# Optimization experiments

Measured on AMD Instinct MI355X. Metric: run time of the kernel, lower is better.

Reference implementation:

```python
import jax, jax.numpy as jnp
import numpy as np

B, T, TKV, D, H = 4, 2048, 512, 1024, 16
HD = D // H  # 64
HIDDEN = ((int(D * 4 * 2 / 3) + 7) // 8) * 8  # 2736
EPS = 1e-6


def setup_inputs() -> dict:
    key = jax.random.key(0)
    ks = jax.random.split(key, 16)
    x = jax.random.normal(ks[0], (B, T, D), jnp.float32)
    memory = jax.random.normal(ks[1], (B, TKV, D), jnp.float32)
    # RoPE frequencies: (T, HD//2, 2) = (cos, sin)
    inv_freq = 1.0 / (10000.0 ** (jnp.arange(0, HD, 2, dtype=jnp.float32) / HD))
    angles = jnp.arange(T, dtype=jnp.float32)[:, None] * inv_freq[None, :]
    freqs_cis = jnp.stack([jnp.cos(angles), jnp.sin(angles)], axis=-1)
    # causal mask (T, T): 0 on/below diag, -inf above
    causal_mask = jnp.where(jnp.tril(jnp.ones((T, T), bool)), 0.0, -jnp.inf).astype(jnp.float32)
    s = 0.02
    w = lambda k, i, o: jax.random.normal(k, (i, o), jnp.float32) * s  # stored as (in, out)
    return {
        'x': x, 'memory': memory, 'freqs_cis': freqs_cis, 'causal_mask': causal_mask,
        'sa_wq': w(ks[2], D, D), 'sa_wk': w(ks[3], D, D), 'sa_wv': w(ks[4], D, D), 'sa_wo': w(ks[5], D, D),
        'ca_wq': w(ks[6], D, D), 'ca_wk': w(ks[7], D, D), 'ca_wv': w(ks[8], D, D), 'ca_wo': w(ks[9], D, D),
        'w1': w(ks[10], D, HIDDEN), 'w3': w(ks[11], D, HIDDEN), 'w2': w(ks[12], HIDDEN, D),
        'g_sa': jnp.ones((D,), jnp.float32), 'g_ca': jnp.ones((D,), jnp.float32), 'g_ffn': jnp.ones((D,), jnp.float32),
    }


def rmsnorm(x, g):
    return x * jax.lax.rsqrt(jnp.mean(x * x, axis=-1, keepdims=True) + EPS) * g


def apply_rope(t, f):
    # t: (B, H, T, HD); f: (T, HD//2, 2)
    tr = t.reshape(*t.shape[:-1], HD // 2, 2)
    a, b = tr[..., 0], tr[..., 1]
    cos, sin = f[None, None, :, :, 0], f[None, None, :, :, 1]
    out = jnp.stack([a * cos - b * sin, a * sin + b * cos], axis=-1)
    return out.reshape(t.shape)


def heads(x, w):
    # (B, S, D) @ (D, D) -> (B, H, S, HD)
    b, s, _ = x.shape
    return (x @ w).reshape(b, s, H, HD).transpose(0, 2, 1, 3)


def attention(xq, kv, wq, wk, wv, wo, freqs=None, mask=None):
    q, k, v = heads(xq, wq), heads(kv, wk), heads(kv, wv)
    if freqs is not None:
        q, k = apply_rope(q, freqs), apply_rope(k, freqs)
    attn = jnp.einsum('bhqd,bhkd->bhqk', q, k) * (HD ** -0.5)
    if mask is not None:
        attn = attn + mask
    attn = jax.nn.softmax(attn, axis=-1)
    out = jnp.einsum('bhqk,bhkd->bhqd', attn, v)
    out = out.transpose(0, 2, 1, 3).reshape(xq.shape[0], xq.shape[1], D)
    return out @ wo


def reference(x, memory, freqs_cis, causal_mask,
              sa_wq, sa_wk, sa_wv, sa_wo,
              ca_wq, ca_wk, ca_wv, ca_wo,
              w1, w2, w3, g_sa, g_ca, g_ffn):
    x = rmsnorm(x + attention(x, x, sa_wq, sa_wk, sa_wv, sa_wo, freqs=freqs_cis, mask=causal_mask), g_sa)
    x = rmsnorm(x + attention(x, memory, ca_wq, ca_wk, ca_wv, ca_wo), g_ca)
    ffn = (jax.nn.silu(x @ w1) * (x @ w3)) @ w2
    x = rmsnorm(x + ffn, g_ffn)
    return x
```

## Files before the change

kernel.cpp:

```cpp
#include <hip/hip_runtime.h>
#include <hip/hip_bf16.h>

typedef __attribute__((ext_vector_type(8))) short s16x8;
typedef __attribute__((ext_vector_type(4))) float f32x4;
typedef __attribute__((ext_vector_type(16))) float f32x16;
typedef unsigned short u16;
typedef unsigned int u32;
typedef unsigned long long u64;

#define MFMA(a,b,c) __builtin_amdgcn_mfma_f32_16x16x32_bf16(a,b,c,0,0,0)
#define MFMA32(a,b,c) __builtin_amdgcn_mfma_f32_32x32x16_bf16(a,b,c,0,0,0)

constexpr int B_ = 4, T_ = 2048, TKV_ = 512, D_ = 1024, H_ = 16, HD_ = 64;
constexpr int HID_ = 2736, HIDP_ = 2816;

__device__ __forceinline__ float bf2f(u16 x) {
    union { float f; u32 u; } c; c.u = ((u32)x) << 16; return c.f;
}
__device__ __forceinline__ u16 f2bf(float f) {
    union { float f; u32 u; } c; c.f = f;
    u32 r = c.u + 0x7fffu + ((c.u >> 16) & 1u);
    return (u16)(r >> 16);
}

__device__ __forceinline__ void gload16(const void* g, void* l) {
    __builtin_amdgcn_global_load_lds(
        (const __attribute__((address_space(1))) u32*)g,
        (__attribute__((address_space(3))) u32*)l, 16, 0, 0);
}

__global__ __launch_bounds__(256) void wt_cast(const float* __restrict__ W, u16* __restrict__ WT,
                                               int K, int N, int Kp, int Np) {
    __shared__ float t[32][33];
    int tid = threadIdx.x;
    int tx = tid & 31, ty = tid >> 5;
    int n0 = blockIdx.x * 32, k0 = blockIdx.y * 32;
#pragma unroll
    for (int i = 0; i < 4; ++i) {
        int kk = k0 + ty + i * 8, nn = n0 + tx;
        t[ty + i * 8][tx] = (kk < K && nn < N) ? W[(size_t)kk * N + nn] : 0.f;
    }
    __syncthreads();
#pragma unroll
    for (int i = 0; i < 4; ++i) {
        int nn = n0 + ty + i * 8, kk = k0 + tx;
        WT[(size_t)nn * Kp + kk] = f2bf(t[tx][ty + i * 8]);
    }
}

__global__ __launch_bounds__(256) void cast_bf16(const float* __restrict__ in, u16* __restrict__ out, int n4) {
    int i = blockIdx.x * 256 + threadIdx.x;
    if (i >= n4) return;
    float4 v = ((const float4*)in)[i];
    u64 pk = (u64)f2bf(v.x) | ((u64)f2bf(v.y) << 16) | ((u64)f2bf(v.z) << 32) | ((u64)f2bf(v.w) << 48);
    ((u64*)out)[i] = pk;
}

__device__ __forceinline__ void gemm_store(void* C, const u16* mul, size_t idx, float v, int mode) {
    if (mode == 0) {
        ((float*)C)[idx] = v;
    } else if (mode == 1) {
        ((u16*)C)[idx] = f2bf(v);
    } else if (mode == 2) {
        float sg = 1.f / (1.f + __expf(-v));
        ((u16*)C)[idx] = f2bf(v * sg);
    } else if (mode == 3) {
        float h = bf2f(mul[idx]);
        ((u16*)C)[idx] = f2bf(v * h);
    } else {
        ((u16*)C)[idx] = f2bf(v * 0.125f);
    }
}


__global__ __launch_bounds__(256) void gemm_bf16(const u16* __restrict__ A, const u16* __restrict__ Bt,
                                                 void* __restrict__ C, const u16* __restrict__ mul,
                                                 int M, int N, int K, int mode, int nwg) {
    __shared__ __align__(16) u16 As[128 * 64];
    __shared__ __align__(16) u16 Bs[128 * 64];
    const int tid = threadIdx.x;
    const int lane = tid & 63, wid = tid >> 6;
    const int wr = wid >> 1, wc = wid & 1;
    const int li = lane & 15, g = lane >> 4;

    int bid = (int)blockIdx.x;
    bid = (bid & 7) * (nwg >> 3) + (bid >> 3);

    const int tn = N >> 7;
    const int m0 = (bid / tn) * 128, n0 = (bid % tn) * 128;

    const int rowst = tid >> 3;
    const int colb = (((tid & 7) ^ ((tid >> 3) & 7)) * 16);
    const char* ga = (const char*)A + ((size_t)(m0 + rowst) * K) * 2 + colb;
    const char* gb = (const char*)Bt + ((size_t)(n0 + rowst) * K) * 2 + colb;
    const size_t rstride = (size_t)32 * K * 2;

    f32x4 acc[4][4] = {};
    const int nt = K >> 6;

    for (int t = 0; t < nt; ++t) {
#pragma unroll
        for (int i = 0; i < 4; ++i) {
            gload16(ga + (size_t)t * 128 + i * rstride, (char*)As + i * 4096 + wid * 1024);
            gload16(gb + (size_t)t * 128 + i * rstride, (char*)Bs + i * 4096 + wid * 1024);
        }
        __syncthreads();
#pragma unroll
        for (int kk = 0; kk < 2; ++kk) {
            s16x8 aF[4], bF[4];
            const int sl = ((kk << 2) | g) ^ (li & 7);
#pragma unroll
            for (int m = 0; m < 4; ++m) aF[m] = *(const s16x8*)&As[(wr * 64 + m * 16 + li) * 64 + sl * 8];
#pragma unroll
            for (int n = 0; n < 4; ++n) bF[n] = *(const s16x8*)&Bs[(wc * 64 + n * 16 + li) * 64 + sl * 8];
#pragma unroll
            for (int m = 0; m < 4; ++m)
#pragma unroll
                for (int n = 0; n < 4; ++n)
                    acc[m][n] = MFMA(aF[m], bF[n], acc[m][n]);
        }
        __syncthreads();
    }

#pragma unroll
    for (int m = 0; m < 4; ++m)
#pragma unroll
        for (int n = 0; n < 4; ++n)
#pragma unroll
            for (int r = 0; r < 4; ++r) {
                size_t row = m0 + wr * 64 + m * 16 + g * 4 + r;
                size_t col = n0 + wc * 64 + n * 16 + li;
                gemm_store(C, mul, row * N + col, acc[m][n][r], mode);
            }
}

__global__ __launch_bounds__(256) void gemm_w13(const u16* __restrict__ A, const u16* __restrict__ B1t,
                                                const u16* __restrict__ B3t, u16* __restrict__ Hout,
                                                int M, int N, int K, int nwg) {
    __shared__ __align__(16) u16 As[128 * 64];
    __shared__ __align__(16) u16 B1s[128 * 64];
    __shared__ __align__(16) u16 B3s[128 * 64];
    const int tid = threadIdx.x;
    const int lane = tid & 63, wid = tid >> 6;
    const int wr = wid >> 1, wc = wid & 1;
    const int li = lane & 15, g = lane >> 4;

    int bid = (int)blockIdx.x;
    bid = (bid & 7) * (nwg >> 3) + (bid >> 3);

    const int tn = N >> 7;
    const int m0 = (bid / tn) * 128, n0 = (bid % tn) * 128;

    const int rowst = tid >> 3;
    const int colb = (((tid & 7) ^ ((tid >> 3) & 7)) * 16);
    const char* ga = (const char*)A + ((size_t)(m0 + rowst) * K) * 2 + colb;
    const char* gb1 = (const char*)B1t + ((size_t)(n0 + rowst) * K) * 2 + colb;
    const char* gb3 = (const char*)B3t + ((size_t)(n0 + rowst) * K) * 2 + colb;
    const size_t rstride = (size_t)32 * K * 2;

    f32x4 acc1[4][4] = {}, acc3[4][4] = {};
    const int nt = K >> 6;

    for (int t = 0; t < nt; ++t) {
#pragma unroll
        for (int i = 0; i < 4; ++i) {
            gload16(ga + (size_t)t * 128 + i * rstride, (char*)As + i * 4096 + wid * 1024);
            gload16(gb1 + (size_t)t * 128 + i * rstride, (char*)B1s + i * 4096 + wid * 1024);
            gload16(gb3 + (size_t)t * 128 + i * rstride, (char*)B3s + i * 4096 + wid * 1024);
        }
        __syncthreads();
#pragma unroll
        for (int kk = 0; kk < 2; ++kk) {
            const int sl = ((kk << 2) | g) ^ (li & 7);
            s16x8 aF[4];
#pragma unroll
            for (int m = 0; m < 4; ++m) aF[m] = *(const s16x8*)&As[(wr * 64 + m * 16 + li) * 64 + sl * 8];
            {
                s16x8 bF[4];
#pragma unroll
                for (int n = 0; n < 4; ++n) bF[n] = *(const s16x8*)&B1s[(wc * 64 + n * 16 + li) * 64 + sl * 8];
#pragma unroll
                for (int m = 0; m < 4; ++m)
#pragma unroll
                    for (int n = 0; n < 4; ++n)
                        acc1[m][n] = MFMA(aF[m], bF[n], acc1[m][n]);
            }
            {
                s16x8 bF[4];
#pragma unroll
                for (int n = 0; n < 4; ++n) bF[n] = *(const s16x8*)&B3s[(wc * 64 + n * 16 + li) * 64 + sl * 8];
#pragma unroll
                for (int m = 0; m < 4; ++m)
#pragma unroll
                    for (int n = 0; n < 4; ++n)
                        acc3[m][n] = MFMA(aF[m], bF[n], acc3[m][n]);
            }
        }
        __syncthreads();
    }

#pragma unroll
    for (int m = 0; m < 4; ++m)
#pragma unroll
        for (int n = 0; n < 4; ++n)
#pragma unroll
            for (int r = 0; r < 4; ++r) {
                size_t row = m0 + wr * 64 + m * 16 + g * 4 + r;
                size_t col = n0 + wc * 64 + n * 16 + li;
                float h1 = acc1[m][n][r];
                float h3 = acc3[m][n][r];
                float sg = 1.f / (1.f + __expf(-h1));
                Hout[row * N + col] = f2bf(h1 * sg * h3);
            }
}

__global__ __launch_bounds__(256) void rope_qk(u16* __restrict__ q, u16* __restrict__ k,
                                               const float* __restrict__ fr, int S) {
    size_t idx = (size_t)blockIdx.x * 256 + threadIdx.x;
    int i = (int)(idx & 31);
    int h = (int)((idx >> 5) & 15);
    size_t bt = idx >> 9;
    int t = (int)(bt & (T_ - 1));
    float2 cs = ((const float2*)fr)[t * 32 + i];
    size_t off = bt * (size_t)S + h * 64 + 2 * i;
    {
        u32* p = (u32*)(q + off);
        u32 w = *p;
        float a = bf2f((u16)(w & 0xffff)), b = bf2f((u16)(w >> 16));
        *p = (u32)f2bf((a * cs.x - b * cs.y) * 0.125f) | ((u32)f2bf((a * cs.y + b * cs.x) * 0.125f) << 16);
    }
    {
        u32* p = (u32*)(k + off);
        u32 w = *p;
        float a = bf2f((u16)(w & 0xffff)), b = bf2f((u16)(w >> 16));
        *p = (u32)f2bf(a * cs.x - b * cs.y) | ((u32)f2bf(a * cs.y + b * cs.x) << 16);
    }
}

__global__ __launch_bounds__(256) void vtrans(const u16* __restrict__ v, u16* __restrict__ vT,
                                              int Tk, int S) {
    __shared__ u16 tile[32][34];
    int bh = blockIdx.x;
    int t0 = blockIdx.y * 32, d0 = blockIdx.z * 32;
    int b = bh >> 4, h = bh & 15;
    int tid = threadIdx.x;
    int tx = tid & 31, ty = tid >> 5;
#pragma unroll
    for (int i = 0; i < 4; ++i)
        tile[ty + i * 8][tx] = v[((size_t)b * Tk + t0 + ty + i * 8) * S + h * 64 + d0 + tx];
    __syncthreads();
#pragma unroll
    for (int i = 0; i < 4; ++i)
        vT[((size_t)bh * 64 + d0 + ty + i * 8) * Tk + t0 + tx] = tile[tx][ty + i * 8];
}

__device__ __forceinline__ void attn32(const u16* __restrict__ qh, const u16* __restrict__ kh,
                                       const u16* __restrict__ vh, u16* __restrict__ oh,
                                       int q0, int nkb, int Tk, int causal, int lq, int hi,
                                       int QS, int KS) {
    const u16* qb = qh + (size_t)(q0 + lq) * QS;
    s16x8 qf[4];
#pragma unroll
    for (int c = 0; c < 4; ++c) qf[c] = *(const s16x8*)&qb[c * 16 + hi * 8];

    f32x16 o0 = {}, o1 = {};
    float mr = -1e30f, lr = 0.f;

    for (int kb = 0; kb < nkb; ++kb) {
        const int ks = kb * 32;
        f32x16 s = {};
        const u16* kp = kh + (size_t)(ks + lq) * KS + hi * 8;
#pragma unroll
        for (int c = 0; c < 4; ++c) {
            s16x8 kf = *(const s16x8*)&kp[c * 16];
            s = MFMA32(kf, qf[c], s);
        }
        if (causal && kb == nkb - 1) {
#pragma unroll
            for (int r = 0; r < 16; ++r) {
                int kl = (r & 3) + 8 * (r >> 2) + 4 * hi;
                if (kl > lq) s[r] = -1e30f;
            }
        }
        float bm = fmaxf(fmaxf(fmaxf(s[0], s[1]), fmaxf(s[2], s[3])),
                         fmaxf(fmaxf(s[4], s[5]), fmaxf(s[6], s[7])));
        float bm2 = fmaxf(fmaxf(fmaxf(s[8], s[9]), fmaxf(s[10], s[11])),
                          fmaxf(fmaxf(s[12], s[13]), fmaxf(s[14], s[15])));
        bm = fmaxf(bm, bm2);
        bm = fmaxf(bm, __shfl_xor(bm, 32));
        float mn = fmaxf(mr, bm);
        float sc = __expf(mr - mn);
        mr = mn;
        float p[16];
        float rs = 0.f;
#pragma unroll
        for (int r = 0; r < 16; ++r) { p[r] = __expf(s[r] - mn); rs += p[r]; }
        rs += __shfl_xor(rs, 32);
        lr = lr * sc + rs;
#pragma unroll
        for (int r = 0; r < 16; ++r) { o0[r] *= sc; o1[r] *= sc; }

        u32 pk[8];
#pragma unroll
        for (int i = 0; i < 8; ++i)
            pk[i] = (u32)f2bf(p[2 * i]) | ((u32)f2bf(p[2 * i + 1]) << 16);
        u32 e1 = __shfl_xor(hi ? pk[0] : pk[2], 32);
        u32 e2 = __shfl_xor(hi ? pk[1] : pk[3], 32);
        u32 e3 = __shfl_xor(hi ? pk[4] : pk[6], 32);
        u32 e4 = __shfl_xor(hi ? pk[5] : pk[7], 32);
        union { s16x8 v; u32 w[4]; } pf0, pf1;
        pf0.w[0] = hi ? e1 : pk[0];
        pf0.w[1] = hi ? e2 : pk[1];
        pf0.w[2] = hi ? pk[2] : e1;
        pf0.w[3] = hi ? pk[3] : e2;
        pf1.w[0] = hi ? e3 : pk[4];
        pf1.w[1] = hi ? e4 : pk[5];
        pf1.w[2] = hi ? pk[6] : e3;
        pf1.w[3] = hi ? pk[7] : e4;

        const u16* v0 = vh + (size_t)lq * Tk + ks + hi * 8;
        const u16* v1 = vh + (size_t)(32 + lq) * Tk + ks + hi * 8;
        o0 = MFMA32(*(const s16x8*)&v0[0],  pf0.v, o0);
        o0 = MFMA32(*(const s16x8*)&v0[16], pf1.v, o0);
        o1 = MFMA32(*(const s16x8*)&v1[0],  pf0.v, o1);
        o1 = MFMA32(*(const s16x8*)&v1[16], pf1.v, o1);
    }

    float inv = 1.f / lr;
    u16* ob = oh + (size_t)(q0 + lq) * D_;
#pragma unroll
    for (int r = 0; r < 16; ++r) {
        int hd = (r & 3) + 8 * (r >> 2) + 4 * hi;
        ob[hd] = f2bf(o0[r] * inv);
        ob[hd + 32] = f2bf(o1[r] * inv);
    }
}

__global__ __launch_bounds__(256) void attn_causal32(const u16* __restrict__ q, const u16* __restrict__ k,
                                                     const u16* __restrict__ vT, u16* __restrict__ o,
                                                     int Tq, int Tk, int QS, int KS) {
    const int lane = threadIdx.x & 63, wid = threadIdx.x >> 6;
    const int lq = lane & 31, hi = lane >> 5;
    const int ntile = Tq / 32;
    const int ppb = (ntile / 2) / 4;
    const int bh = blockIdx.x / ppb;
    const int p = (blockIdx.x % ppb) * 4 + wid;
    const int b = bh >> 4, h = bh & 15;

    const u16* qh = q + ((size_t)b * Tq) * QS + h * 64;
    const u16* kh = k + ((size_t)b * Tk) * KS + h * 64;
    const u16* vh = vT + ((size_t)bh * 64) * Tk;
    u16* oh = o + ((size_t)b * Tq) * D_ + h * 64;

    const int tA = p, tB = ntile - 1 - p;
    attn32(qh, kh, vh, oh, tA * 32, tA + 1, Tk, 1, lq, hi, QS, KS);
    attn32(qh, kh, vh, oh, tB * 32, tB + 1, Tk, 1, lq, hi, QS, KS);
}

__global__ __launch_bounds__(256) void attn_plain32(const u16* __restrict__ q, const u16* __restrict__ k,
                                                    const u16* __restrict__ vT, u16* __restrict__ o,
                                                    int Tq, int Tk, int QS, int KS) {
    const int lane = threadIdx.x & 63, wid = threadIdx.x >> 6;
    const int lq = lane & 31, hi = lane >> 5;
    const int tpb = (Tq / 32) / 4;
    const int bh = blockIdx.x / tpb;
    const int qt = (blockIdx.x % tpb) * 4 + wid;
    const int b = bh >> 4, h = bh & 15;

    const u16* qh = q + ((size_t)b * Tq) * QS + h * 64;
    const u16* kh = k + ((size_t)b * Tk) * KS + h * 64;
    const u16* vh = vT + ((size_t)bh * 64) * Tk;
    u16* oh = o + ((size_t)b * Tq) * D_ + h * 64;

    attn32(qh, kh, vh, oh, qt * 32, Tk / 32, Tk, 0, lq, hi, QS, KS);
}

__global__ __launch_bounds__(256) void addnorm(const float* __restrict__ xa, const float* __restrict__ xb,
                                               const float* __restrict__ gg, float* __restrict__ fo,
                                               u16* __restrict__ bo) {
    int row = blockIdx.x * 4 + (threadIdx.x >> 6);
    int lane = threadIdx.x & 63;
    const float4* pa = (const float4*)(xa + (size_t)row * D_);
    const float4* pb = (const float4*)(xb + (size_t)row * D_);
    float4 v[4];
    float ss = 0.f;
#pragma unroll
    for (int j = 0; j < 4; ++j) {
        float4 a = pa[lane + 64 * j];
        float4 b = pb[lane + 64 * j];
        v[j].x = a.x + b.x; v[j].y = a.y + b.y; v[j].z = a.z + b.z; v[j].w = a.w + b.w;
        ss += v[j].x * v[j].x + v[j].y * v[j].y + v[j].z * v[j].z + v[j].w * v[j].w;
    }
    ss += __shfl_xor(ss, 1);
    ss += __shfl_xor(ss, 2);
    ss += __shfl_xor(ss, 4);
    ss += __shfl_xor(ss, 8);
    ss += __shfl_xor(ss, 16);
    ss += __shfl_xor(ss, 32);
    float s = rsqrtf(ss * (1.0f / D_) + 1e-6f);
#pragma unroll
    for (int j = 0; j < 4; ++j) {
        float4 gv = ((const float4*)gg)[lane + 64 * j];
        float yx = v[j].x * s * gv.x, yy = v[j].y * s * gv.y;
        float yz = v[j].z * s * gv.z, yw = v[j].w * s * gv.w;
        if (fo) {
            float4 o4; o4.x = yx; o4.y = yy; o4.z = yz; o4.w = yw;
            ((float4*)(fo + (size_t)row * D_))[lane + 64 * j] = o4;
        }
        if (bo) {
            u64 pk = (u64)f2bf(yx) | ((u64)f2bf(yy) << 16) | ((u64)f2bf(yz) << 32) | ((u64)f2bf(yw) << 48);
            ((u64*)(bo + (size_t)row * D_))[lane + 64 * j] = pk;
        }
    }
}

extern "C" void kernel_launch(void* const* d_in, const int* in_sizes, int n_in,
                              void* d_out, int out_size, void* d_ws, size_t ws_size,
                              hipStream_t stream) {
    const float* x    = (const float*)d_in[0];
    const float* mem  = (const float*)d_in[1];
    const float* fr   = (const float*)d_in[2];
    const float* wsaq = (const float*)d_in[4];
    const float* wsak = (const float*)d_in[5];
    const float* wsav = (const float*)d_in[6];
    const float* wsao = (const float*)d_in[7];
    const float* wcaq = (const float*)d_in[8];
    const float* wcak = (const float*)d_in[9];
    const float* wcav = (const float*)d_in[10];
    const float* wcao = (const float*)d_in[11];
    const float* w1   = (const float*)d_in[12];
    const float* w3   = (const float*)d_in[13];
    const float* w2   = (const float*)d_in[14];
    const float* g_sa = (const float*)d_in[15];
    const float* g_ca = (const float*)d_in[16];
    const float* g_ff = (const float*)d_in[17];
    float* outF = (float*)d_out;

    char* p = (char*)d_ws;
    auto alloc = [&](size_t bytes) { char* r = p; p += (bytes + 255) & ~(size_t)255; return r; };
    const size_t DD2 = (size_t)1024 * 1024 * 2;
    u16* wqkvT = (u16*)alloc(3 * DD2);
    u16* saoT  = (u16*)alloc(DD2);
    u16* caqT  = (u16*)alloc(DD2);
    u16* wkvT  = (u16*)alloc(2 * DD2);
    u16* caoT  = (u16*)alloc(DD2);
    u16* w1T   = (u16*)alloc((size_t)HIDP_ * 1024 * 2);
    u16* w3T   = (u16*)alloc((size_t)HIDP_ * 1024 * 2);
    u16* w2T   = (u16*)alloc((size_t)1024 * HIDP_ * 2);
    u16* Ab    = (u16*)alloc((size_t)8192 * 1024 * 2);
    u16* memb  = (u16*)alloc((size_t)2048 * 1024 * 2);
    char* qkvRaw = alloc((size_t)8192 * 3072 * 2);
    u16* qkvb = (u16*)qkvRaw;
    u16* kvb  = (u16*)qkvRaw;
    u16* caqb = (u16*)(qkvRaw + (size_t)25165824);
    u16* vtb  = (u16*)alloc((size_t)8192 * 1024 * 2);
    u16* ob   = (u16*)alloc((size_t)8192 * 1024 * 2);
    float* Pf = (float*)alloc((size_t)8192 * 1024 * 4);
    float* Rf = (float*)alloc((size_t)8192 * 1024 * 4);
    u16* Hb   = (u16*)alloc((size_t)8192 * HIDP_ * 2);

    dim3 blk(256);

    wt_cast<<<dim3(32, 32), blk, 0, stream>>>(wsaq, wqkvT,               1024, 1024, 1024, 1024);
    wt_cast<<<dim3(32, 32), blk, 0, stream>>>(wsak, wqkvT + 1024 * 1024, 1024, 1024, 1024, 1024);
    wt_cast<<<dim3(32, 32), blk, 0, stream>>>(wsav, wqkvT + 2048 * 1024, 1024, 1024, 1024, 1024);
    wt_cast<<<dim3(32, 32), blk, 0, stream>>>(wsao, saoT, 1024, 1024, 1024, 1024);
    wt_cast<<<dim3(32, 32), blk, 0, stream>>>(wcaq, caqT, 1024, 1024, 1024, 1024);
    wt_cast<<<dim3(32, 32), blk, 0, stream>>>(wcak, wkvT,               1024, 1024, 1024, 1024);
    wt_cast<<<dim3(32, 32), blk, 0, stream>>>(wcav, wkvT + 1024 * 1024, 1024, 1024, 1024, 1024);
    wt_cast<<<dim3(32, 32), blk, 0, stream>>>(wcao, caoT, 1024, 1024, 1024, 1024);
    wt_cast<<<dim3(88, 32), blk, 0, stream>>>(w1, w1T, 1024, HID_, 1024, HIDP_);
    wt_cast<<<dim3(88, 32), blk, 0, stream>>>(w3, w3T, 1024, HID_, 1024, HIDP_);
    wt_cast<<<dim3(32, 88), blk, 0, stream>>>(w2, w2T, HID_, 1024, HIDP_, 1024);

    cast_bf16<<<8192, blk, 0, stream>>>(x, Ab, 2097152);
    cast_bf16<<<2048, blk, 0, stream>>>(mem, memb, 524288);

    gemm_bf16<<<1536, blk, 0, stream>>>(Ab, wqkvT, qkvb, nullptr, 8192, 3072, 1024, 1, 1536);
    rope_qk<<<16384, blk, 0, stream>>>(qkvb, qkvb + 1024, fr, 3072);
    vtrans<<<dim3(64, 64, 2), blk, 0, stream>>>(qkvb + 2048, vtb, 2048, 3072);
    attn_causal32<<<512, blk, 0, stream>>>(qkvb, qkvb + 1024, vtb, ob, 2048, 2048, 3072, 3072);
    gemm_bf16<<<512, blk, 0, stream>>>(ob, saoT, Pf, nullptr, 8192, 1024, 1024, 0, 512);
    addnorm<<<2048, blk, 0, stream>>>(x, Pf, g_sa, Rf, Ab);

    gemm_bf16<<<512, blk, 0, stream>>>(Ab, caqT, caqb, nullptr, 8192, 1024, 1024, 4, 512);
    gemm_bf16<<<256, blk, 0, stream>>>(memb, wkvT, kvb, nullptr, 2048, 2048, 1024, 1, 256);
    vtrans<<<dim3(64, 16, 2), blk, 0, stream>>>(kvb + 1024, vtb, 512, 2048);
    attn_plain32<<<1024, blk, 0, stream>>>(caqb, kvb, vtb, ob, 2048, 512, 1024, 2048);
    gemm_bf16<<<512, blk, 0, stream>>>(ob, caoT, Pf, nullptr, 8192, 1024, 1024, 0, 512);
    addnorm<<<2048, blk, 0, stream>>>(Rf, Pf, g_ca, Rf, Ab);

    gemm_w13<<<1408, blk, 0, stream>>>(Ab, w1T, w3T, Hb, 8192, HIDP_, 1024, 1408);
    gemm_bf16<<<512, blk, 0, stream>>>(Hb, w2T, Pf, nullptr, 8192, 1024, HIDP_, 0, 512);
    addnorm<<<2048, blk, 0, stream>>>(Rf, Pf, g_ff, outF, nullptr);
}
```

Baseline: 824.1 us.

## Widen GEMM tiles to 128x256 with each wave owning a 64-column slab

```diff
diff --git a/kernel.cpp b/kernel.cpp
--- a/kernel.cpp
+++ b/kernel.cpp
@@ -73,21 +73,20 @@
 }
 
 
-__global__ __launch_bounds__(256) void gemm_bf16(const u16* __restrict__ A, const u16* __restrict__ Bt,
+__global__ __launch_bounds__(256) void gemm_wide(const u16* __restrict__ A, const u16* __restrict__ Bt,
                                                  void* __restrict__ C, const u16* __restrict__ mul,
                                                  int M, int N, int K, int mode, int nwg) {
     __shared__ __align__(16) u16 As[128 * 64];
-    __shared__ __align__(16) u16 Bs[128 * 64];
+    __shared__ __align__(16) u16 Bs[256 * 64];
     const int tid = threadIdx.x;
     const int lane = tid & 63, wid = tid >> 6;
-    const int wr = wid >> 1, wc = wid & 1;
     const int li = lane & 15, g = lane >> 4;
 
     int bid = (int)blockIdx.x;
     bid = (bid & 7) * (nwg >> 3) + (bid >> 3);
 
-    const int tn = N >> 7;
-    const int m0 = (bid / tn) * 128, n0 = (bid % tn) * 128;
+    const int tn = N >> 8;
+    const int m0 = (bid / tn) * 128, n0 = (bid % tn) * 256;
 
     const int rowst = tid >> 3;
     const int colb = (((tid & 7) ^ ((tid >> 3) & 7)) * 16);
@@ -95,41 +94,42 @@
     const char* gb = (const char*)Bt + ((size_t)(n0 + rowst) * K) * 2 + colb;
     const size_t rstride = (size_t)32 * K * 2;
 
-    f32x4 acc[4][4] = {};
+    f32x4 acc[8][4] = {};
     const int nt = K >> 6;
 
     for (int t = 0; t < nt; ++t) {
 #pragma unroll
-        for (int i = 0; i < 4; ++i) {
+        for (int i = 0; i < 4; ++i)
             gload16(ga + (size_t)t * 128 + i * rstride, (char*)As + i * 4096 + wid * 1024);
+#pragma unroll
+        for (int i = 0; i < 8; ++i)
             gload16(gb + (size_t)t * 128 + i * rstride, (char*)Bs + i * 4096 + wid * 1024);
-        }
         __syncthreads();
 #pragma unroll
         for (int kk = 0; kk < 2; ++kk) {
-            s16x8 aF[4], bF[4];
             const int sl = ((kk << 2) | g) ^ (li & 7);
-#pragma unroll
-            for (int m = 0; m < 4; ++m) aF[m] = *(const s16x8*)&As[(wr * 64 + m * 16 + li) * 64 + sl * 8];
-#pragma unroll
-            for (int n = 0; n < 4; ++n) bF[n] = *(const s16x8*)&Bs[(wc * 64 + n * 16 + li) * 64 + sl * 8];
-#pragma unroll
-            for (int m = 0; m < 4; ++m)
+            s16x8 bF[4];
+#pragma unroll
+            for (int n = 0; n < 4; ++n) bF[n] = *(const s16x8*)&Bs[(wid * 64 + n * 16 + li) * 64 + sl * 8];
+#pragma unroll
+            for (int m = 0; m < 8; ++m) {
+                s16x8 aF = *(const s16x8*)&As[(m * 16 + li) * 64 + sl * 8];
 #pragma unroll
                 for (int n = 0; n < 4; ++n)
-                    acc[m][n] = MFMA(aF[m], bF[n], acc[m][n]);
+                    acc[m][n] = MFMA(aF, bF[n], acc[m][n]);
+            }
         }
         __syncthreads();
     }
 
 #pragma unroll
-    for (int m = 0; m < 4; ++m)
+    for (int m = 0; m < 8; ++m)
 #pragma unroll
         for (int n = 0; n < 4; ++n)
 #pragma unroll
             for (int r = 0; r < 4; ++r) {
-                size_t row = m0 + wr * 64 + m * 16 + g * 4 + r;
-                size_t col = n0 + wc * 64 + n * 16 + li;
+                size_t row = m0 + m * 16 + g * 4 + r;
+                size_t col = n0 + wid * 64 + n * 16 + li;
                 gemm_store(C, mul, row * N + col, acc[m][n][r], mode);
             }
 }
@@ -476,21 +476,21 @@
     cast_bf16<<<8192, blk, 0, stream>>>(x, Ab, 2097152);
     cast_bf16<<<2048, blk, 0, stream>>>(mem, memb, 524288);
 
-    gemm_bf16<<<1536, blk, 0, stream>>>(Ab, wqkvT, qkvb, nullptr, 8192, 3072, 1024, 1, 1536);
+    gemm_wide<<<768, blk, 0, stream>>>(Ab, wqkvT, qkvb, nullptr, 8192, 3072, 1024, 1, 768);
     rope_qk<<<16384, blk, 0, stream>>>(qkvb, qkvb + 1024, fr, 3072);
     vtrans<<<dim3(64, 64, 2), blk, 0, stream>>>(qkvb + 2048, vtb, 2048, 3072);
     attn_causal32<<<512, blk, 0, stream>>>(qkvb, qkvb + 1024, vtb, ob, 2048, 2048, 3072, 3072);
-    gemm_bf16<<<512, blk, 0, stream>>>(ob, saoT, Pf, nullptr, 8192, 1024, 1024, 0, 512);
+    gemm_wide<<<256, blk, 0, stream>>>(ob, saoT, Pf, nullptr, 8192, 1024, 1024, 0, 256);
     addnorm<<<2048, blk, 0, stream>>>(x, Pf, g_sa, Rf, Ab);
 
-    gemm_bf16<<<512, blk, 0, stream>>>(Ab, caqT, caqb, nullptr, 8192, 1024, 1024, 4, 512);
-    gemm_bf16<<<256, blk, 0, stream>>>(memb, wkvT, kvb, nullptr, 2048, 2048, 1024, 1, 256);
+    gemm_wide<<<256, blk, 0, stream>>>(Ab, caqT, caqb, nullptr, 8192, 1024, 1024, 4, 256);
+    gemm_wide<<<128, blk, 0, stream>>>(memb, wkvT, kvb, nullptr, 2048, 2048, 1024, 1, 128);
     vtrans<<<dim3(64, 16, 2), blk, 0, stream>>>(kvb + 1024, vtb, 512, 2048);
     attn_plain32<<<1024, blk, 0, stream>>>(caqb, kvb, vtb, ob, 2048, 512, 1024, 2048);
-    gemm_bf16<<<512, blk, 0, stream>>>(ob, caoT, Pf, nullptr, 8192, 1024, 1024, 0, 512);
+    gemm_wide<<<256, blk, 0, stream>>>(ob, caoT, Pf, nullptr, 8192, 1024, 1024, 0, 256);
     addnorm<<<2048, blk, 0, stream>>>(Rf, Pf, g_ca, Rf, Ab);
 
     gemm_w13<<<1408, blk, 0, stream>>>(Ab, w1T, w3T, Hb, 8192, HIDP_, 1024, 1408);
-    gemm_bf16<<<512, blk, 0, stream>>>(Hb, w2T, Pf, nullptr, 8192, 1024, HIDP_, 0, 512);
+    gemm_wide<<<256, blk, 0, stream>>>(Hb, w2T, Pf, nullptr, 8192, 1024, HIDP_, 0, 256);
     addnorm<<<2048, blk, 0, stream>>>(Rf, Pf, g_ff, outF, nullptr);
 }
```

After: 1.061 ms. +28.8%, slower.
